# Optimization experiments

Measured on AMD Instinct MI355X. Metric: run time of the kernel, lower is better.

The kernel has to match this reference:

```python
import jax, jax.numpy as jnp
import numpy as np

B, F0, D = 4096, 39, 16
CROSS_LAYER_SIZE = (128, 128)


def _he_uniform(key, shape):
    fan_in = int(np.prod(shape[:-1]))
    limit = np.sqrt(6.0 / fan_in)
    return jax.random.uniform(key, shape, jnp.float32, -limit, limit)


def setup_inputs() -> dict:
    key = jax.random.key(0)
    k_x, k_f0, k_f1, k_w, k_b = jax.random.split(key, 5)
    x = jax.random.normal(k_x, (B, F0, D), dtype=jnp.float32)
    # field_nums with direct=False: [39, 128//2=64, 64]
    f0 = _he_uniform(k_f0, (F0 * F0, CROSS_LAYER_SIZE[0]))          # (1521, 128)
    f1 = _he_uniform(k_f1, (F0 * (CROSS_LAYER_SIZE[0] // 2), CROSS_LAYER_SIZE[1]))  # (2496, 128)
    out_dim = CROSS_LAYER_SIZE[0] // 2 + CROSS_LAYER_SIZE[1]        # 192
    dense_w = _he_uniform(k_w, (out_dim, 1))
    dense_b = jnp.zeros((1,), dtype=jnp.float32)
    return {"x": x, "f0": f0, "f1": f1, "dense_w": dense_w, "dense_b": dense_b}


def reference(x, f0, f1, dense_w, dense_b):
    # CIN forward (direct=False, use_bias=False, use_residual=False, relu)
    # x: (B, F0, D)
    filters = [f0, f1]
    n_layers = len(CROSS_LAYER_SIZE)
    h = x  # hidden state, (B, Fk, D)
    finals = []
    for idx, L in enumerate(CROSS_LAYER_SIZE):
        Fk = h.shape[1]
        # filter f_ has shape (F0*Fk, L) with i (field of x0) major, j (field of h) minor
        Wr = filters[idx].reshape(F0, Fk, L)
        # fused outer product + conv1d (kernel width 1 == matmul over i,j):
        # z[b, m, d] = sum_{i,j} x[b,i,d] * h[b,j,d] * W[i,j,m]
        z = jnp.einsum('bid,bjd,ijm->bmd', x, h, Wr)  # (B, L, D)
        z = jax.nn.relu(z)
        if idx != n_layers - 1:
            # split along feature-map axis: first half feeds next layer,
            # second half goes to output
            h = z[:, : L // 2, :]
            finals.append(z[:, L // 2:, :])
        else:
            finals.append(z)
    result = jnp.sum(jnp.concatenate(finals, axis=1), axis=-1)  # (B, 192)
    return result @ dense_w + dense_b  # (B, 1)
```

## Files before the change

kernel.cpp:

```cpp
#include <hip/hip_runtime.h>


typedef _Float16 h2    __attribute__((ext_vector_type(2)));
typedef _Float16 f16x8 __attribute__((ext_vector_type(8)));
typedef __attribute__((ext_vector_type(16))) float f32x16;

#define XBB 1160
#define L0C 30
#define NCH 110

__device__ __constant__ int IG0[L0C] = {0,0,0,0,0, 1,1,1,1,1, 2,2,2,2, 3,3,3,3, 4,4,4, 5,5,5, 6,6, 7,7, 8, 9};
__device__ __constant__ int JG0[L0C] = {0,1,2,3,4, 0,1,2,3,4, 1,2,3,4, 1,2,3,4, 2,3,4, 2,3,4, 3,4, 3,4, 4, 4};
#define IG0T(c) ((c)<5?0:(c)<10?1:(c)<14?2:(c)<18?3:(c)<21?4:(c)<24?5:(c)<26?6:(c)<28?7:(c)<29?8:9)
#define JG0T(c) ((c)<10?((c)%5):(c)<18?(((c)-10)%4+1):(c)<24?(((c)-18)%3+2):(c)<28?(((c)-24)%2+3):4)

__global__ __launch_bounds__(256)
void CIN_repack(const float* __restrict__ f0, const float* __restrict__ f1,
                uint4* __restrict__ ws)
{
    const int tid  = blockIdx.x * 256 + threadIdx.x;
    const int n    = tid & 127;
    const int slot = tid >> 7;
    const int half = slot & 1;
    const int kh   = (slot >> 1) & 1;
    const int ch   = slot >> 2;
    float v[8];
    if (ch < L0C) {
        const int ig = IG0[ch], jg = JG0[ch];
        const int i = ig * 4 + kh * 2 + half;
#pragma unroll
        for (int t = 0; t < 8; ++t) {
            const int j = jg * 8 + t;
            float val = 0.f;
            if (i < 39 && j < 39 && j >= i) {
                val = f0[(i * 39 + j) * 128 + n];
                if (j > i) val += f0[(j * 39 + i) * 128 + n];
            }
            v[t] = val;
        }
    } else {
        const int c1 = ch - L0C;
        const int jg = c1 / 5, ig = c1 - jg * 5;
        const int j = jg * 4 + kh * 2 + half;
#pragma unroll
        for (int t = 0; t < 8; ++t) {
            const int i = ig * 8 + t;
            v[t] = (i < 39) ? f1[(i * 64 + j) * 128 + n] : 0.f;
        }
    }
    union { h2 h[4]; uint4 q; } pk;
#pragma unroll
    for (int t = 0; t < 4; ++t)
        pk.h[t] = h2{(_Float16)v[2 * t], (_Float16)v[2 * t + 1]};
    const int lane = half * 32 + (n & 31);
    const int cg   = n >> 5;
    ws[ch * 512 + kh * 256 + cg * 64 + lane] = pk.q;
}

__global__ __launch_bounds__(256, 2)
void CIN_main(const float* __restrict__ x,
              const char* __restrict__ wsB,
              const float* __restrict__ dw,
              const float* __restrict__ db,
              float* __restrict__ out)
{
    __shared__ __align__(16) char bBc[4 * 8192];
    __shared__ __align__(16) _Float16 xsH[8 * XBB];
    __shared__ __align__(4)  _Float16 hsH[8][64][18];
    __shared__ float dws[192];
    __shared__ float red[4][4];

    const int tid  = threadIdx.x;
    const int w    = tid >> 6;
    const int wp   = w >> 1;
    const int wn   = w & 1;
    const int lane = tid & 63;
    const int half = lane >> 5;
    const int d    = lane & 15;
    const int bsel = (lane >> 4) & 1;
    const int col  = lane & 31;

    auto stageB = [&](int ch, int buf) {
        const char* src = wsB + (size_t)ch * 8192 + w * 2048 + lane * 16;
        char* dst = bBc + buf * 8192 + w * 2048;
        __builtin_amdgcn_global_load_lds(
            (const __attribute__((address_space(1))) void*)(src),
            (__attribute__((address_space(3))) void*)(dst), 16, 0, 0);
        __builtin_amdgcn_global_load_lds(
            (const __attribute__((address_space(1))) void*)(src + 1024),
            (__attribute__((address_space(3))) void*)(dst + 1024), 16, 0, 0);
    };

    stageB(0, 0);
    stageB(1, 1);

    const float4* xg4 = (const float4*)(x + (size_t)blockIdx.x * 8 * 624);
    for (int e4 = tid; e4 < 1248; e4 += 256) {
        float4 v = xg4[e4];
        int bb = e4 / 156, r = e4 - bb * 156;
        int i = r >> 2, d0 = (r & 3) * 4;
        _Float16* bp = xsH + bb * XBB + i;
        bp[(d0 + 0) * 72] = (_Float16)v.x; bp[(d0 + 1) * 72] = (_Float16)v.y;
        bp[(d0 + 2) * 72] = (_Float16)v.z; bp[(d0 + 3) * 72] = (_Float16)v.w;
    }
    if (tid < 128) { int bb = tid >> 4, dd = tid & 15; xsH[bb * XBB + dd * 72 + 39] = (_Float16)0.f; }
    if (tid < 192) dws[tid] = dw[tid];
    __syncthreads();

    const _Float16* xrow[2] = {
        xsH + ((wp * 2 + 0) * 2 + bsel) * XBB + d * 72,
        xsH + ((wp * 2 + 1) * 2 + bsel) * XBB + d * 72
    };

    h2 xw[2][20];
#pragma unroll
    for (int p = 0; p < 2; ++p)
#pragma unroll
        for (int w5 = 0; w5 < 5; ++w5) {
            union { f16x8 v; h2 h[4]; } u;
            u.v = *(const f16x8*)(xrow[p] + w5 * 8);
#pragma unroll
            for (int q = 0; q < 4; ++q) xw[p][w5 * 4 + q] = u.h[q];
        }

    f32x16 acc[2][2];
#pragma unroll
    for (int p = 0; p < 2; ++p)
#pragma unroll
        for (int nq = 0; nq < 2; ++nq)
#pragma unroll
            for (int r = 0; r < 16; ++r) acc[p][nq][r] = 0.f;

    h2 sp2[2][2];
    const char* bfr = bBc + wn * 2048 + (size_t)lane * 16;

#pragma unroll
    for (int c = 0; c < L0C; ++c) {
        asm volatile("s_waitcnt vmcnt(2)" ::: "memory");
        __builtin_amdgcn_sched_barrier(0);
        __builtin_amdgcn_s_barrier();
        const int ig = IG0T(c);
        const int jg = JG0T(c);
        if ((c == 0) || (IG0T(c) != IG0T(c - 1))) {
#pragma unroll
            for (int p = 0; p < 2; ++p)
#pragma unroll
                for (int kh = 0; kh < 2; ++kh) {
                    const h2 pr = xw[p][ig * 2 + kh];
                    const _Float16 vv = half ? pr.y : pr.x;
                    sp2[p][kh] = h2{vv, vv};
                }
        }
        const char* bb = bfr + (c & 3) * 8192;
        const f16x8 B00 = *(const f16x8*)(bb);
        const f16x8 B01 = *(const f16x8*)(bb + 1024);
        const f16x8 B10 = *(const f16x8*)(bb + 4096);
        const f16x8 B11 = *(const f16x8*)(bb + 5120);
        stageB(c + 2, (c + 2) & 3);
#pragma unroll
        for (int p = 0; p < 2; ++p) {
            union { h2 h[4]; f16x8 v; } a0, a1;
#pragma unroll
            for (int q = 0; q < 4; ++q) {
                a0.h[q] = sp2[p][0] * xw[p][jg * 4 + q];
                a1.h[q] = sp2[p][1] * xw[p][jg * 4 + q];
            }
            acc[p][0] = __builtin_amdgcn_mfma_f32_32x32x16_f16(a0.v, B00, acc[p][0], 0, 0, 0);
            acc[p][1] = __builtin_amdgcn_mfma_f32_32x32x16_f16(a0.v, B01, acc[p][1], 0, 0, 0);
            acc[p][0] = __builtin_amdgcn_mfma_f32_32x32x16_f16(a1.v, B10, acc[p][0], 0, 0, 0);
            acc[p][1] = __builtin_amdgcn_mfma_f32_32x32x16_f16(a1.v, B11, acc[p][1], 0, 0, 0);
        }
    }

    float cs[4] = {0.f, 0.f, 0.f, 0.f};
    if (wn == 0) {
#pragma unroll
        for (int p = 0; p < 2; ++p)
#pragma unroll
            for (int nq = 0; nq < 2; ++nq)
#pragma unroll
                for (int r = 0; r < 16; r += 2) {
                    const int row = (r & 3) + 8 * (r >> 2) + 4 * half;
                    h2 pr = h2{(_Float16)fmaxf(acc[p][nq][r],     0.f),
                               (_Float16)fmaxf(acc[p][nq][r + 1], 0.f)};
                    *(h2*)&hsH[(wp * 2 + p) * 2 + (row >> 4)][nq * 32 + col][row & 15] = pr;
                }
    } else {
#pragma unroll
        for (int nq = 0; nq < 2; ++nq) {
            const float dwv = dws[nq * 32 + col];
#pragma unroll
            for (int p = 0; p < 2; ++p)
#pragma unroll
                for (int r = 0; r < 16; ++r) {
                    const int row = (r & 3) + 8 * (r >> 2) + 4 * half;
                    cs[p * 2 + (row >> 4)] += fmaxf(acc[p][nq][r], 0.f) * dwv;
                }
        }
    }
#pragma unroll
    for (int p = 0; p < 2; ++p)
#pragma unroll
        for (int nq = 0; nq < 2; ++nq)
#pragma unroll
            for (int r = 0; r < 16; ++r) acc[p][nq][r] = 0.f;
    __syncthreads();

#pragma unroll 1
    for (int o2 = 0; o2 < 4; ++o2) {
#pragma unroll
        for (int u = 0; u < 20; ++u) {
            asm volatile("s_waitcnt vmcnt(2)" ::: "memory");
            __builtin_amdgcn_sched_barrier(0);
            __builtin_amdgcn_s_barrier();
            const int ig2 = u % 5;
            if (ig2 == 0) {
                const int jb = (o2 * 4 + u / 5) * 4;
#pragma unroll
                for (int p = 0; p < 2; ++p)
#pragma unroll
                    for (int kh = 0; kh < 2; ++kh) {
                        const _Float16 s = hsH[(wp * 2 + p) * 2 + bsel][jb + kh * 2 + half][d];
                        sp2[p][kh] = h2{s, s};
                    }
            }
            const char* bb = bfr + ((2 + u) & 3) * 8192;
            const f16x8 B00 = *(const f16x8*)(bb);
            const f16x8 B01 = *(const f16x8*)(bb + 1024);
            const f16x8 B10 = *(const f16x8*)(bb + 4096);
            const f16x8 B11 = *(const f16x8*)(bb + 5120);
            int chn = 30 + o2 * 20 + u + 2; if (chn > NCH - 1) chn = NCH - 1;
            stageB(chn, u & 3);
#pragma unroll
            for (int p = 0; p < 2; ++p) {
                union { h2 h[4]; f16x8 v; } a0, a1;
#pragma unroll
                for (int q = 0; q < 4; ++q) {
                    a0.h[q] = sp2[p][0] * xw[p][ig2 * 4 + q];
                    a1.h[q] = sp2[p][1] * xw[p][ig2 * 4 + q];
                }
                acc[p][0] = __builtin_amdgcn_mfma_f32_32x32x16_f16(a0.v, B00, acc[p][0], 0, 0, 0);
                acc[p][1] = __builtin_amdgcn_mfma_f32_32x32x16_f16(a0.v, B01, acc[p][1], 0, 0, 0);
                acc[p][0] = __builtin_amdgcn_mfma_f32_32x32x16_f16(a1.v, B10, acc[p][0], 0, 0, 0);
                acc[p][1] = __builtin_amdgcn_mfma_f32_32x32x16_f16(a1.v, B11, acc[p][1], 0, 0, 0);
            }
        }
    }

#pragma unroll
    for (int nq = 0; nq < 2; ++nq) {
        const float dwv = dws[64 + (wn * 2 + nq) * 32 + col];
#pragma unroll
        for (int p = 0; p < 2; ++p)
#pragma unroll
            for (int r = 0; r < 16; ++r) {
                const int row = (r & 3) + 8 * (r >> 2) + 4 * half;
                cs[p * 2 + (row >> 4)] += fmaxf(acc[p][nq][r], 0.f) * dwv;
            }
    }
#pragma unroll
    for (int rr = 0; rr < 4; ++rr)
#pragma unroll
        for (int off = 32; off > 0; off >>= 1)
            cs[rr] += __shfl_xor(cs[rr], off, 64);
    if (lane == 0) {
#pragma unroll
        for (int rr = 0; rr < 4; ++rr) red[w][rr] = cs[rr];
    }
    __syncthreads();
    if (tid < 8) {
        const int wpp = tid >> 2, l = tid & 3;
        out[blockIdx.x * 8 + tid] = red[wpp * 2][l] + red[wpp * 2 + 1][l] + db[0];
    }
}

extern "C" void kernel_launch(void* const* d_in, const int* in_sizes, int n_in,
                              void* d_out, int out_size, void* d_ws, size_t ws_size,
                              hipStream_t stream)
{
    const float* x  = (const float*)d_in[0];
    const float* f0 = (const float*)d_in[1];
    const float* f1 = (const float*)d_in[2];
    const float* dw = (const float*)d_in[3];
    const float* db = (const float*)d_in[4];
    float* out = (float*)d_out;

    CIN_repack<<<dim3(220), dim3(256), 0, stream>>>(f0, f1, (uint4*)d_ws);
    CIN_main<<<dim3(512), dim3(256), 0, stream>>>(x, (const char*)d_ws, dw, db, out);
}
```

Measured before the change: 120.3 us.

## Deepen weight staging ring to five buffers and split MFMA accumulator chains

Grows the LDS ring of B-weight chunks from four to five slots and prefetches four chunks ahead instead of two, relaxing the vmcnt wait so more global-to-LDS loads are in flight. It also splits each accumulator into two independent chains, one per k-half, so consecutive MFMAs no longer depend on each other's result, and sums the two chains in the epilogue. The cost is more LDS per block (extra 8 KB), double the accumulator registers (64 more VGPRs/AGPRs), which may hurt occupancy at 2 blocks per CU, and modulo-5 buffer indexing.

```diff
diff --git a/kernel.cpp b/kernel.cpp
--- a/kernel.cpp
+++ b/kernel.cpp
@@ -64,7 +64,7 @@
               const float* __restrict__ db,
               float* __restrict__ out)
 {
-    __shared__ __align__(16) char bBc[4 * 8192];
+    __shared__ __align__(16) char bBc[5 * 8192];
     __shared__ __align__(16) _Float16 xsH[8 * XBB];
     __shared__ __align__(4)  _Float16 hsH[8][64][18];
     __shared__ float dws[192];
@@ -93,6 +93,8 @@
 
     stageB(0, 0);
     stageB(1, 1);
+    stageB(2, 2);
+    stageB(3, 3);
 
     const float4* xg4 = (const float4*)(x + (size_t)blockIdx.x * 8 * 624);
     for (int e4 = tid; e4 < 1248; e4 += 256) {
@@ -123,20 +125,22 @@
             for (int q = 0; q < 4; ++q) xw[p][w5 * 4 + q] = u.h[q];
         }
 
-    f32x16 acc[2][2];
-#pragma unroll
-    for (int p = 0; p < 2; ++p)
-#pragma unroll
-        for (int nq = 0; nq < 2; ++nq)
-#pragma unroll
-            for (int r = 0; r < 16; ++r) acc[p][nq][r] = 0.f;
+    f32x16 acc[2][2][2];
+#pragma unroll
+    for (int kh = 0; kh < 2; ++kh)
+#pragma unroll
+        for (int p = 0; p < 2; ++p)
+#pragma unroll
+            for (int nq = 0; nq < 2; ++nq)
+#pragma unroll
+                for (int r = 0; r < 16; ++r) acc[kh][p][nq][r] = 0.f;
 
     h2 sp2[2][2];
     const char* bfr = bBc + wn * 2048 + (size_t)lane * 16;
 
 #pragma unroll
     for (int c = 0; c < L0C; ++c) {
-        asm volatile("s_waitcnt vmcnt(2)" ::: "memory");
+        asm volatile("s_waitcnt vmcnt(6)" ::: "memory");
         __builtin_amdgcn_sched_barrier(0);
         __builtin_amdgcn_s_barrier();
         const int ig = IG0T(c);
@@ -151,12 +155,12 @@
                     sp2[p][kh] = h2{vv, vv};
                 }
         }
-        const char* bb = bfr + (c & 3) * 8192;
+        const char* bb = bfr + (c % 5) * 8192;
         const f16x8 B00 = *(const f16x8*)(bb);
         const f16x8 B01 = *(const f16x8*)(bb + 1024);
         const f16x8 B10 = *(const f16x8*)(bb + 4096);
         const f16x8 B11 = *(const f16x8*)(bb + 5120);
-        stageB(c + 2, (c + 2) & 3);
+        stageB(c + 4, (c + 4) % 5);
 #pragma unroll
         for (int p = 0; p < 2; ++p) {
             union { h2 h[4]; f16x8 v; } a0, a1;
@@ -165,10 +169,10 @@
                 a0.h[q] = sp2[p][0] * xw[p][jg * 4 + q];
                 a1.h[q] = sp2[p][1] * xw[p][jg * 4 + q];
             }
-            acc[p][0] = __builtin_amdgcn_mfma_f32_32x32x16_f16(a0.v, B00, acc[p][0], 0, 0, 0);
-            acc[p][1] = __builtin_amdgcn_mfma_f32_32x32x16_f16(a0.v, B01, acc[p][1], 0, 0, 0);
-            acc[p][0] = __builtin_amdgcn_mfma_f32_32x32x16_f16(a1.v, B10, acc[p][0], 0, 0, 0);
-            acc[p][1] = __builtin_amdgcn_mfma_f32_32x32x16_f16(a1.v, B11, acc[p][1], 0, 0, 0);
+            acc[0][p][0] = __builtin_amdgcn_mfma_f32_32x32x16_f16(a0.v, B00, acc[0][p][0], 0, 0, 0);
+            acc[0][p][1] = __builtin_amdgcn_mfma_f32_32x32x16_f16(a0.v, B01, acc[0][p][1], 0, 0, 0);
+            acc[1][p][0] = __builtin_amdgcn_mfma_f32_32x32x16_f16(a1.v, B10, acc[1][p][0], 0, 0, 0);
+            acc[1][p][1] = __builtin_amdgcn_mfma_f32_32x32x16_f16(a1.v, B11, acc[1][p][1], 0, 0, 0);
         }
     }
 
@@ -181,8 +185,8 @@
 #pragma unroll
                 for (int r = 0; r < 16; r += 2) {
                     const int row = (r & 3) + 8 * (r >> 2) + 4 * half;
-                    h2 pr = h2{(_Float16)fmaxf(acc[p][nq][r],     0.f),
-                               (_Float16)fmaxf(acc[p][nq][r + 1], 0.f)};
+                    h2 pr = h2{(_Float16)fmaxf(acc[0][p][nq][r]     + acc[1][p][nq][r],     0.f),
+                               (_Float16)fmaxf(acc[0][p][nq][r + 1] + acc[1][p][nq][r + 1], 0.f)};
                     *(h2*)&hsH[(wp * 2 + p) * 2 + (row >> 4)][nq * 32 + col][row & 15] = pr;
                 }
     } else {
@@ -194,23 +198,25 @@
 #pragma unroll
                 for (int r = 0; r < 16; ++r) {
                     const int row = (r & 3) + 8 * (r >> 2) + 4 * half;
-                    cs[p * 2 + (row >> 4)] += fmaxf(acc[p][nq][r], 0.f) * dwv;
-                }
-        }
-    }
-#pragma unroll
-    for (int p = 0; p < 2; ++p)
-#pragma unroll
-        for (int nq = 0; nq < 2; ++nq)
-#pragma unroll
-            for (int r = 0; r < 16; ++r) acc[p][nq][r] = 0.f;
+                    cs[p * 2 + (row >> 4)] += fmaxf(acc[0][p][nq][r] + acc[1][p][nq][r], 0.f) * dwv;
+                }
+        }
+    }
+#pragma unroll
+    for (int kh = 0; kh < 2; ++kh)
+#pragma unroll
+        for (int p = 0; p < 2; ++p)
+#pragma unroll
+            for (int nq = 0; nq < 2; ++nq)
+#pragma unroll
+                for (int r = 0; r < 16; ++r) acc[kh][p][nq][r] = 0.f;
     __syncthreads();
 
 #pragma unroll 1
     for (int o2 = 0; o2 < 4; ++o2) {
 #pragma unroll
         for (int u = 0; u < 20; ++u) {
-            asm volatile("s_waitcnt vmcnt(2)" ::: "memory");
+            asm volatile("s_waitcnt vmcnt(6)" ::: "memory");
             __builtin_amdgcn_sched_barrier(0);
             __builtin_amdgcn_s_barrier();
             const int ig2 = u % 5;
@@ -224,13 +230,13 @@
                         sp2[p][kh] = h2{s, s};
                     }
             }
-            const char* bb = bfr + ((2 + u) & 3) * 8192;
+            const char* bb = bfr + (u % 5) * 8192;
             const f16x8 B00 = *(const f16x8*)(bb);
             const f16x8 B01 = *(const f16x8*)(bb + 1024);
             const f16x8 B10 = *(const f16x8*)(bb + 4096);
             const f16x8 B11 = *(const f16x8*)(bb + 5120);
-            int chn = 30 + o2 * 20 + u + 2; if (chn > NCH - 1) chn = NCH - 1;
-            stageB(chn, u & 3);
+            int sn = 30 + o2 * 20 + u + 4; if (sn > NCH - 1) sn = NCH - 1;
+            stageB(sn, (u + 4) % 5);
 #pragma unroll
             for (int p = 0; p < 2; ++p) {
                 union { h2 h[4]; f16x8 v; } a0, a1;
@@ -239,10 +245,10 @@
                     a0.h[q] = sp2[p][0] * xw[p][ig2 * 4 + q];
                     a1.h[q] = sp2[p][1] * xw[p][ig2 * 4 + q];
                 }
-                acc[p][0] = __builtin_amdgcn_mfma_f32_32x32x16_f16(a0.v, B00, acc[p][0], 0, 0, 0);
-                acc[p][1] = __builtin_amdgcn_mfma_f32_32x32x16_f16(a0.v, B01, acc[p][1], 0, 0, 0);
-                acc[p][0] = __builtin_amdgcn_mfma_f32_32x32x16_f16(a1.v, B10, acc[p][0], 0, 0, 0);
-                acc[p][1] = __builtin_amdgcn_mfma_f32_32x32x16_f16(a1.v, B11, acc[p][1], 0, 0, 0);
+                acc[0][p][0] = __builtin_amdgcn_mfma_f32_32x32x16_f16(a0.v, B00, acc[0][p][0], 0, 0, 0);
+                acc[0][p][1] = __builtin_amdgcn_mfma_f32_32x32x16_f16(a0.v, B01, acc[0][p][1], 0, 0, 0);
+                acc[1][p][0] = __builtin_amdgcn_mfma_f32_32x32x16_f16(a1.v, B10, acc[1][p][0], 0, 0, 0);
+                acc[1][p][1] = __builtin_amdgcn_mfma_f32_32x32x16_f16(a1.v, B11, acc[1][p][1], 0, 0, 0);
             }
         }
     }
@@ -255,7 +261,7 @@
 #pragma unroll
             for (int r = 0; r < 16; ++r) {
                 const int row = (r & 3) + 8 * (r >> 2) + 4 * half;
-                cs[p * 2 + (row >> 4)] += fmaxf(acc[p][nq][r], 0.f) * dwv;
+                cs[p * 2 + (row >> 4)] += fmaxf(acc[0][p][nq][r] + acc[1][p][nq][r], 0.f) * dwv;
             }
     }
 #pragma unroll
```

Result: no change. 118.4 us (-1.6%).
